# Optimization experiments

Hardware: AMD Instinct MI355X
Metric: run time of the kernel (lower is better)

Reference implementation:

```python
import jax, jax.numpy as jnp
import numpy as np

B, N, H_IN, H_HID, N_HEAD = 32, 500, 64, 16, 8
N_VALID = 400  # valid (non-padded) nodes per graph; node 0 is the root
NEG_INF = -1e20


def setup_inputs() -> dict:
    key = jax.random.key(0)
    ks = jax.random.split(key, 10)
    x = jax.random.normal(ks[0], (B, N, H_IN), jnp.float32)
    # sparse-ish binary adjacency with self loops
    A = (jax.random.uniform(ks[1], (B, N, N)) < 0.05).astype(jnp.float32)
    A = jnp.maximum(A, jnp.eye(N, dtype=jnp.float32)[None])
    # mask_nonzero: first N_VALID nodes of every graph are valid
    mask_batch = jnp.repeat(jnp.arange(B, dtype=jnp.int32), N_VALID)
    mask_row = jnp.tile(jnp.arange(N_VALID, dtype=jnp.int32), B)
    s = 0.1
    w1 = jax.random.normal(ks[2], (N_HEAD, H_IN, H_HID), jnp.float32) * s
    a_src1 = jax.random.normal(ks[3], (N_HEAD, H_HID), jnp.float32) * s
    a_dst1 = jax.random.normal(ks[4], (N_HEAD, H_HID), jnp.float32) * s
    w2 = jax.random.normal(ks[5], (1, N_HEAD * H_HID, H_IN), jnp.float32) * s
    a_src2 = jax.random.normal(ks[6], (1, H_IN), jnp.float32) * s
    a_dst2 = jax.random.normal(ks[7], (1, H_IN), jnp.float32) * s
    attn_w = jax.random.normal(ks[8], (2 * H_IN,), jnp.float32) * s
    return {"x": x, "A": A, "mask_batch": mask_batch, "mask_row": mask_row,
            "w1": w1, "a_src1": a_src1, "a_dst1": a_dst1,
            "w2": w2, "a_src2": a_src2, "a_dst2": a_dst2, "attn_w": attn_w}


def gat_layer(h_in, A, w, a_src, a_dst):
    # h_in: [B,N,F_in]; w: [H,F_in,F_out]
    h = jnp.einsum('bnf,hfo->bhno', h_in, w)              # [B,H,N,F_out]
    e_src = jnp.einsum('bhno,ho->bhn', h, a_src)          # [B,H,N]
    e_dst = jnp.einsum('bhno,ho->bhn', h, a_dst)
    e = jax.nn.leaky_relu(e_src[..., :, None] + e_dst[..., None, :], 0.2)  # [B,H,N,N]
    e = jnp.where(A[:, None, :, :] > 0, e, NEG_INF)
    attn = jax.nn.softmax(e, axis=-1)
    return jnp.einsum('bhnm,bhmo->bhno', attn, h)         # [B,H,N,F_out]


def reference(x, A, mask_batch, mask_row, w1, a_src1, a_dst1, w2, a_src2, a_dst2, attn_w):
    b, n, _ = x.shape
    # BatchGAT encoder: layer 1 (multi-head, concat + ELU), layer 2 (1 head -> h_in)
    h1 = gat_layer(x, A, w1, a_src1, a_dst1)                       # [B,H,N,h_hid]
    h1 = jax.nn.elu(h1).transpose(0, 2, 1, 3).reshape(b, n, -1)    # [B,N,H*h_hid]
    xc = gat_layer(h1, A, w2, a_src2, a_dst2)[:, 0]                # [B,N,h_in]
    # zero out padded nodes (so their Post_Attn scores are exactly 0)
    valid = jnp.zeros((b, n), x.dtype).at[mask_batch, mask_row].set(1.0)
    xc = xc * valid[:, :, None]
    # Post_Attn: scatter root features to each valid node position
    root = jnp.zeros_like(xc).at[mask_batch, mask_row, :].set(xc[mask_batch, 0, :])
    x_plus = jnp.concatenate([xc, root], axis=-1)                  # [B,N,2*h_in]
    score = x_plus @ attn_w                                        # [B,N]
    score = jnp.where(score == 0, NEG_INF, score)[:, :, None]      # masked_fill
    attn = jax.nn.softmax(score, axis=1)                           # softmax over nodes
    pooled = jnp.einsum('bnf,bn->bf', xc, attn[:, :, 0])           # [B,h_in]
    return pooled, attn
```

## Files before the change

### kernel.cpp

```cpp
#include <hip/hip_runtime.h>

#define NB 32
#define NN 500
#define HIN 64
#define HHID 16
#define NHEAD 8
#define NVALID 400
#define MAXK 128
#define NEG_INF -1e20f

__global__ __launch_bounds__(256) void k_nbr(const float* __restrict__ A,
                                             int* __restrict__ nbr, int* __restrict__ cnt)
{
    int row = blockIdx.x * 4 + (threadIdx.x >> 6);
    int lane = threadIdx.x & 63;
    if (row >= NB * NN) return;
    const float* arow = A + (size_t)row * NN;
    int c = 0;
    for (int it = 0; it < 8; ++it) {
        int m = it * 64 + lane;
        bool v = (m < NN) && (arow[m] > 0.0f);
        unsigned long long bal = __ballot(v);
        if (v) {
            int pos = c + __popcll(bal & ((1ull << lane) - 1ull));
            if (pos < MAXK) nbr[(size_t)row * MAXK + pos] = m;
        }
        c += (int)__popcll(bal);
    }
    if (lane == 0) cnt[row] = c < MAXK ? c : MAXK;
}

__global__ __launch_bounds__(256) void k_proj1(const float* __restrict__ x, const float* __restrict__ w1,
                                               const float* __restrict__ as1, const float* __restrict__ ad1,
                                               float* __restrict__ h1p, float* __restrict__ e1s,
                                               float* __restrict__ e1d)
{
    int b = blockIdx.y, chunk = blockIdx.x;
    int t = threadIdx.x, slot = t >> 7, lane = t & 127;
    int h = lane >> 4, o = lane & 15;
    float wreg[64];
#pragma unroll
    for (int f = 0; f < 64; ++f) wreg[f] = w1[h * 1024 + f * 16 + o];
    float as_r = as1[h * 16 + o], ad_r = ad1[h * 16 + o];
    __shared__ __align__(16) float xs[2][64];
    for (int i = 0; i < 8; ++i) {
        int n = chunk * 16 + i * 2 + slot;
        bool valid = n < NN;
        if (valid && lane < 64) xs[slot][lane] = x[(size_t)(b * NN + n) * HIN + lane];
        __syncthreads();
        if (valid) {
            float acc = 0.f;
#pragma unroll
            for (int f4 = 0; f4 < 16; ++f4) {
                float4 xv = *(const float4*)&xs[slot][f4 * 4];
                acc += xv.x * wreg[f4 * 4] + xv.y * wreg[f4 * 4 + 1]
                     + xv.z * wreg[f4 * 4 + 2] + xv.w * wreg[f4 * 4 + 3];
            }
            h1p[((size_t)(b * NHEAD + h) * NN + n) * HHID + o] = acc;
            float vs = acc * as_r, vd = acc * ad_r;
#pragma unroll
            for (int m = 1; m < 16; m <<= 1) { vs += __shfl_xor(vs, m); vd += __shfl_xor(vd, m); }
            if (o == 0) {
                e1s[(size_t)(b * NHEAD + h) * NN + n] = vs;
                e1d[(size_t)(b * NHEAD + h) * NN + n] = vd;
            }
        }
        __syncthreads();
    }
}

__global__ __launch_bounds__(128) void k_agg1(const int* __restrict__ nbr, const int* __restrict__ cnt,
                                              const float* __restrict__ h1p, const float* __restrict__ e1s,
                                              const float* __restrict__ e1d, float* __restrict__ h1cat)
{
    int row = blockIdx.x;
    int b = row / NN, n = row - b * NN;
    int t = threadIdx.x;
    __shared__ int nb_s[MAXK];
    __shared__ float p_s[NHEAD][MAXK];
    __shared__ float stat[NHEAD][2];
    int K = cnt[row];
    for (int k = t; k < K; k += 128) nb_s[k] = nbr[(size_t)row * MAXK + k];
    __syncthreads();
    for (int idx = t; idx < NHEAD * K; idx += 128) {
        int h = idx / K, k = idx - h * K;
        float e = e1s[(size_t)(b * NHEAD + h) * NN + n]
                + e1d[(size_t)(b * NHEAD + h) * NN + nb_s[k]];
        p_s[h][k] = e > 0.f ? e : 0.2f * e;
    }
    __syncthreads();
    if (t < NHEAD) {
        float mx = -1e30f;
        for (int k = 0; k < K; ++k) mx = fmaxf(mx, p_s[t][k]);
        float sum = 0.f;
        for (int k = 0; k < K; ++k) sum += __expf(p_s[t][k] - mx);
        stat[t][0] = mx; stat[t][1] = 1.f / sum;
    }
    __syncthreads();
    for (int idx = t; idx < NHEAD * K; idx += 128) {
        int h = idx / K, k = idx - h * K;
        p_s[h][k] = __expf(p_s[h][k] - stat[h][0]) * stat[h][1];
    }
    __syncthreads();
    int h = t >> 4, o = t & 15;
    float acc = 0.f;
    const float* hp = h1p + (size_t)(b * NHEAD + h) * NN * HHID + o;
    for (int k = 0; k < K; ++k) acc += p_s[h][k] * hp[(size_t)nb_s[k] * HHID];
    float outv = acc > 0.f ? acc : expm1f(acc);
    h1cat[(size_t)row * (NHEAD * HHID) + t] = outv;
}

__global__ __launch_bounds__(256) void k_proj2(const float* __restrict__ h1cat, const float* __restrict__ w2,
                                               const float* __restrict__ as2, const float* __restrict__ ad2,
                                               float* __restrict__ h2p, float* __restrict__ e2s,
                                               float* __restrict__ e2d)
{
    int b = blockIdx.y, chunk = blockIdx.x;
    int t = threadIdx.x, slot = t >> 7, lane = t & 127;
    int fh = lane >> 6, o = lane & 63;
    float wreg[64];
#pragma unroll
    for (int j = 0; j < 64; ++j) wreg[j] = w2[(fh * 64 + j) * 64 + o];
    float as_r = as2[o], ad_r = ad2[o];
    __shared__ __align__(16) float xs[2][128];
    __shared__ float part[2][128];
    for (int i = 0; i < 8; ++i) {
        int n = chunk * 16 + i * 2 + slot;
        bool valid = n < NN;
        if (valid) xs[slot][lane] = h1cat[(size_t)(b * NN + n) * 128 + lane];
        __syncthreads();
        float acc = 0.f;
        if (valid) {
#pragma unroll
            for (int j4 = 0; j4 < 16; ++j4) {
                float4 xv = *(const float4*)&xs[slot][fh * 64 + j4 * 4];
                acc += xv.x * wreg[j4 * 4] + xv.y * wreg[j4 * 4 + 1]
                     + xv.z * wreg[j4 * 4 + 2] + xv.w * wreg[j4 * 4 + 3];
            }
        }
        part[slot][lane] = acc;
        __syncthreads();
        if (valid && fh == 0) {
            float val = acc + part[slot][64 + o];
            h2p[(size_t)(b * NN + n) * 64 + o] = val;
            float vs = val * as_r, vd = val * ad_r;
#pragma unroll
            for (int m = 1; m < 64; m <<= 1) { vs += __shfl_xor(vs, m); vd += __shfl_xor(vd, m); }
            if (o == 0) { e2s[b * NN + n] = vs; e2d[b * NN + n] = vd; }
        }
        __syncthreads();
    }
}

__global__ __launch_bounds__(64) void k_agg2(const int* __restrict__ nbr, const int* __restrict__ cnt,
                                             const float* __restrict__ h2p, const float* __restrict__ e2s,
                                             const float* __restrict__ e2d, const float* __restrict__ aw,
                                             float* __restrict__ xc, float* __restrict__ sc,
                                             float* __restrict__ root_dot)
{
    int row = blockIdx.x;
    int b = row / NN, n = row - b * NN;
    int t = threadIdx.x;
    if (n >= NVALID) { xc[(size_t)row * 64 + t] = 0.f; return; }
    __shared__ int nb_s[MAXK];
    __shared__ float p_s[MAXK];
    __shared__ float stat[2];
    int K = cnt[row];
    for (int k = t; k < K; k += 64) nb_s[k] = nbr[(size_t)row * MAXK + k];
    __syncthreads();
    float es = e2s[row];
    for (int k = t; k < K; k += 64) {
        float e = es + e2d[b * NN + nb_s[k]];
        p_s[k] = e > 0.f ? e : 0.2f * e;
    }
    __syncthreads();
    if (t == 0) {
        float mx = -1e30f;
        for (int k = 0; k < K; ++k) mx = fmaxf(mx, p_s[k]);
        float sum = 0.f;
        for (int k = 0; k < K; ++k) sum += __expf(p_s[k] - mx);
        stat[0] = mx; stat[1] = 1.f / sum;
    }
    __syncthreads();
    for (int k = t; k < K; k += 64) p_s[k] = __expf(p_s[k] - stat[0]) * stat[1];
    __syncthreads();
    float acc = 0.f;
    for (int k = 0; k < K; ++k) acc += p_s[k] * h2p[(size_t)(b * NN + nb_s[k]) * 64 + t];
    xc[(size_t)row * 64 + t] = acc;
    float v = acc * aw[t];
#pragma unroll
    for (int m = 1; m < 64; m <<= 1) v += __shfl_xor(v, m);
    if (t == 0) sc[row] = v;
    if (n == 0) {
        float v2 = acc * aw[64 + t];
#pragma unroll
        for (int m = 1; m < 64; m <<= 1) v2 += __shfl_xor(v2, m);
        if (t == 0) root_dot[b] = v2;
    }
}

__global__ __launch_bounds__(1024) void k_pool(const float* __restrict__ xc, const float* __restrict__ sc,
                                               const float* __restrict__ root_dot, float* __restrict__ out)
{
    int b = blockIdx.x;
    int t = threadIdx.x, w = t >> 6, lane = t & 63;
    __shared__ float attn_s[NN];
    __shared__ float red[16];
    __shared__ float part[16][64];
    const float* xb = xc + (size_t)b * NN * 64;
    float rd = root_dot[b];
    float s = NEG_INF;
    if (t < NVALID) {
        s = sc[b * NN + t] + rd;
        if (s == 0.f) s = NEG_INF;
    }
    float mx = s;
#pragma unroll
    for (int m = 1; m < 64; m <<= 1) mx = fmaxf(mx, __shfl_xor(mx, m));
    if (lane == 0) red[w] = mx;
    __syncthreads();
    mx = red[0];
#pragma unroll
    for (int i = 1; i < 16; ++i) mx = fmaxf(mx, red[i]);
    float e = (t < NN) ? __expf(s - mx) : 0.f;
    float sum = e;
#pragma unroll
    for (int m = 1; m < 64; m <<= 1) sum += __shfl_xor(sum, m);
    __syncthreads();
    if (lane == 0) red[w] = sum;
    __syncthreads();
    sum = 0.f;
#pragma unroll
    for (int i = 0; i < 16; ++i) sum += red[i];
    float inv = 1.f / sum;
    if (t < NN) {
        float a = e * inv;
        out[NB * 64 + b * NN + t] = a;
        attn_s[t] = a;
    }
    __syncthreads();
    float acc = 0.f;
    for (int n = w; n < NN; n += 16) acc += attn_s[n] * xb[(size_t)n * 64 + lane];
    part[w][lane] = acc;
    __syncthreads();
    if (t < 64) {
        float v = 0.f;
#pragma unroll
        for (int i = 0; i < 16; ++i) v += part[i][t];
        out[b * 64 + t] = v;
    }
}

extern "C" void kernel_launch(void* const* d_in, const int* in_sizes, int n_in,
                              void* d_out, int out_size, void* d_ws, size_t ws_size,
                              hipStream_t stream) {
    const float* x   = (const float*)d_in[0];
    const float* A   = (const float*)d_in[1];
    const float* w1  = (const float*)d_in[4];
    const float* as1 = (const float*)d_in[5];
    const float* ad1 = (const float*)d_in[6];
    const float* w2  = (const float*)d_in[7];
    const float* as2 = (const float*)d_in[8];
    const float* ad2 = (const float*)d_in[9];
    const float* aw  = (const float*)d_in[10];
    float* out = (float*)d_out;

    char* ws = (char*)d_ws;
    int* nbr = (int*)ws;
    int* cnt = (int*)(ws + (size_t)16000 * 128 * 4);
    float* f = (float*)(ws + (size_t)16000 * 129 * 4);
    float* h1p   = f;  f += (size_t)NB * NHEAD * NN * HHID;
    float* e1s   = f;  f += (size_t)NB * NHEAD * NN;
    float* e1d   = f;  f += (size_t)NB * NHEAD * NN;
    float* h1cat = f;  f += (size_t)NB * NN * 128;
    float* h2p   = f;  f += (size_t)NB * NN * 64;
    float* e2s   = f;  f += (size_t)NB * NN;
    float* e2d   = f;  f += (size_t)NB * NN;
    float* xc    = f;  f += (size_t)NB * NN * 64;
    float* sc    = f;  f += (size_t)NB * NN;
    float* rootd = f;  f += NB;

    hipLaunchKernelGGL(k_nbr,   dim3(4000),   dim3(256), 0, stream, A, nbr, cnt);
    hipLaunchKernelGGL(k_proj1, dim3(32, NB), dim3(256), 0, stream, x, w1, as1, ad1, h1p, e1s, e1d);
    hipLaunchKernelGGL(k_agg1,  dim3(NB * NN), dim3(128), 0, stream, nbr, cnt, h1p, e1s, e1d, h1cat);
    hipLaunchKernelGGL(k_proj2, dim3(32, NB), dim3(256), 0, stream, h1cat, w2, as2, ad2, h2p, e2s, e2d);
    hipLaunchKernelGGL(k_agg2,  dim3(NB * NN), dim3(64), 0, stream, nbr, cnt, h2p, e2s, e2d, aw, xc, sc, rootd);
    hipLaunchKernelGGL(k_pool,  dim3(NB),     dim3(1024), 0, stream, xc, sc, rootd, out);
}
```

Baseline: 186.2 us.

## Fuse all six GAT stages into one cooperative persistent kernel with grid syncs

```diff
diff --git a/kernel.cpp b/kernel.cpp
--- a/kernel.cpp
+++ b/kernel.cpp
@@ -1,4 +1,7 @@
 #include <hip/hip_runtime.h>
+#include <hip/hip_cooperative_groups.h>
+
+namespace cg = cooperative_groups;
 
 #define NB 32
 #define NN 500
@@ -8,54 +11,69 @@
 #define NVALID 400
 #define MAXK 128
 #define NEG_INF -1e20f
-
-__global__ __launch_bounds__(256) void k_nbr(const float* __restrict__ A,
-                                             int* __restrict__ nbr, int* __restrict__ cnt)
+#define GRID 256
+#define BLK 512
+
+union SMem {
+    struct { int nb[8][MAXK]; float p[8][NHEAD][MAXK]; float inv[8][NHEAD]; } a1;
+    struct { int nb[8][MAXK]; float p[8][MAXK]; } a2;
+    struct { float attn[NN]; float red[8]; float part[8][64]; } pl;
+};
+
+__global__ __launch_bounds__(BLK, 2) void k_fused(
+    const float* __restrict__ x, const float* __restrict__ A,
+    const float* __restrict__ w1, const float* __restrict__ as1, const float* __restrict__ ad1,
+    const float* __restrict__ w2, const float* __restrict__ as2, const float* __restrict__ ad2,
+    const float* __restrict__ aw,
+    int* __restrict__ nbr, int* __restrict__ cnt,
+    float* __restrict__ h1p, float* __restrict__ e1s, float* __restrict__ e1d,
+    float* __restrict__ h1cat, float* __restrict__ h2p,
+    float* __restrict__ e2s, float* __restrict__ e2d,
+    float* __restrict__ xc, float* __restrict__ sc, float* __restrict__ rootd,
+    float* __restrict__ out)
 {
-    int row = blockIdx.x * 4 + (threadIdx.x >> 6);
-    int lane = threadIdx.x & 63;
-    if (row >= NB * NN) return;
-    const float* arow = A + (size_t)row * NN;
-    int c = 0;
-    for (int it = 0; it < 8; ++it) {
-        int m = it * 64 + lane;
-        bool v = (m < NN) && (arow[m] > 0.0f);
-        unsigned long long bal = __ballot(v);
-        if (v) {
-            int pos = c + __popcll(bal & ((1ull << lane) - 1ull));
-            if (pos < MAXK) nbr[(size_t)row * MAXK + pos] = m;
-        }
-        c += (int)__popcll(bal);
-    }
-    if (lane == 0) cnt[row] = c < MAXK ? c : MAXK;
-}
-
-__global__ __launch_bounds__(256) void k_proj1(const float* __restrict__ x, const float* __restrict__ w1,
-                                               const float* __restrict__ as1, const float* __restrict__ ad1,
-                                               float* __restrict__ h1p, float* __restrict__ e1s,
-                                               float* __restrict__ e1d)
-{
-    int b = blockIdx.y, chunk = blockIdx.x;
-    int t = threadIdx.x, slot = t >> 7, lane = t & 127;
-    int h = lane >> 4, o = lane & 15;
-    float wreg[64];
-#pragma unroll
-    for (int f = 0; f < 64; ++f) wreg[f] = w1[h * 1024 + f * 16 + o];
-    float as_r = as1[h * 16 + o], ad_r = ad1[h * 16 + o];
-    __shared__ __align__(16) float xs[2][64];
-    for (int i = 0; i < 8; ++i) {
-        int n = chunk * 16 + i * 2 + slot;
-        bool valid = n < NN;
-        if (valid && lane < 64) xs[slot][lane] = x[(size_t)(b * NN + n) * HIN + lane];
-        __syncthreads();
-        if (valid) {
-            float acc = 0.f;
-#pragma unroll
-            for (int f4 = 0; f4 < 16; ++f4) {
-                float4 xv = *(const float4*)&xs[slot][f4 * 4];
-                acc += xv.x * wreg[f4 * 4] + xv.y * wreg[f4 * 4 + 1]
-                     + xv.z * wreg[f4 * 4 + 2] + xv.w * wreg[f4 * 4 + 3];
-            }
+    cg::grid_group gg = cg::this_grid();
+    int t = threadIdx.x, wv = t >> 6, lane = t & 63;
+    __shared__ SMem sm;
+
+    for (int row = blockIdx.x * 8 + wv; row < NB * NN; row += GRID * 8) {
+        const float* ar = A + (size_t)row * NN;
+        int c = 0;
+        for (int it = 0; it < 8; ++it) {
+            int m = it * 64 + lane;
+            bool v = (m < NN) && (ar[m] > 0.f);
+            unsigned long long bal = __ballot(v);
+            if (v) {
+                int pos = c + __popcll(bal & ((1ull << lane) - 1ull));
+                if (pos < MAXK) nbr[(size_t)row * MAXK + pos] = m;
+            }
+            c += (int)__popcll(bal);
+        }
+        if (lane == 0) cnt[row] = c < MAXK ? c : MAXK;
+    }
+    gg.sync();
+
+    {
+        int g = t >> 7, gl = t & 127;
+        int unit = blockIdx.x * 4 + g;
+        int b = unit >> 5, chunk = unit & 31;
+        int h = (gl >> 4) & 7, o = gl & 15;
+        float wreg[64];
+#pragma unroll
+        for (int f = 0; f < 64; ++f) wreg[f] = w1[h * 1024 + f * 16 + o];
+        float as_r = as1[h * 16 + o], ad_r = ad1[h * 16 + o];
+        for (int i = 0; i < 16; ++i) {
+            int n = chunk * 16 + i;
+            if (n >= NN) break;
+            const float4* xp = (const float4*)(x + (size_t)(b * NN + n) * HIN);
+            float a0 = 0.f, a1 = 0.f;
+#pragma unroll
+            for (int f4 = 0; f4 < 16; f4 += 2) {
+                float4 u = xp[f4], v = xp[f4 + 1];
+                a0 += u.x * wreg[f4 * 4] + u.y * wreg[f4 * 4 + 1] + u.z * wreg[f4 * 4 + 2] + u.w * wreg[f4 * 4 + 3];
+                a1 += v.x * wreg[f4 * 4 + 4] + v.y * wreg[f4 * 4 + 5] + v.z * wreg[f4 * 4 + 6] + v.w * wreg[f4 * 4 + 7];
+            }
+            float acc = a0 + a1;
             h1p[((size_t)(b * NHEAD + h) * NN + n) * HHID + o] = acc;
             float vs = acc * as_r, vd = acc * ad_r;
 #pragma unroll
@@ -65,189 +83,184 @@
                 e1d[(size_t)(b * NHEAD + h) * NN + n] = vd;
             }
         }
-        __syncthreads();
-    }
-}
-
-__global__ __launch_bounds__(128) void k_agg1(const int* __restrict__ nbr, const int* __restrict__ cnt,
-                                              const float* __restrict__ h1p, const float* __restrict__ e1s,
-                                              const float* __restrict__ e1d, float* __restrict__ h1cat)
-{
-    int row = blockIdx.x;
-    int b = row / NN, n = row - b * NN;
-    int t = threadIdx.x;
-    __shared__ int nb_s[MAXK];
-    __shared__ float p_s[NHEAD][MAXK];
-    __shared__ float stat[NHEAD][2];
-    int K = cnt[row];
-    for (int k = t; k < K; k += 128) nb_s[k] = nbr[(size_t)row * MAXK + k];
-    __syncthreads();
-    for (int idx = t; idx < NHEAD * K; idx += 128) {
-        int h = idx / K, k = idx - h * K;
-        float e = e1s[(size_t)(b * NHEAD + h) * NN + n]
-                + e1d[(size_t)(b * NHEAD + h) * NN + nb_s[k]];
-        p_s[h][k] = e > 0.f ? e : 0.2f * e;
-    }
-    __syncthreads();
-    if (t < NHEAD) {
-        float mx = -1e30f;
-        for (int k = 0; k < K; ++k) mx = fmaxf(mx, p_s[t][k]);
-        float sum = 0.f;
-        for (int k = 0; k < K; ++k) sum += __expf(p_s[t][k] - mx);
-        stat[t][0] = mx; stat[t][1] = 1.f / sum;
-    }
-    __syncthreads();
-    for (int idx = t; idx < NHEAD * K; idx += 128) {
-        int h = idx / K, k = idx - h * K;
-        p_s[h][k] = __expf(p_s[h][k] - stat[h][0]) * stat[h][1];
-    }
-    __syncthreads();
-    int h = t >> 4, o = t & 15;
-    float acc = 0.f;
-    const float* hp = h1p + (size_t)(b * NHEAD + h) * NN * HHID + o;
-    for (int k = 0; k < K; ++k) acc += p_s[h][k] * hp[(size_t)nb_s[k] * HHID];
-    float outv = acc > 0.f ? acc : expm1f(acc);
-    h1cat[(size_t)row * (NHEAD * HHID) + t] = outv;
-}
-
-__global__ __launch_bounds__(256) void k_proj2(const float* __restrict__ h1cat, const float* __restrict__ w2,
-                                               const float* __restrict__ as2, const float* __restrict__ ad2,
-                                               float* __restrict__ h2p, float* __restrict__ e2s,
-                                               float* __restrict__ e2d)
-{
-    int b = blockIdx.y, chunk = blockIdx.x;
-    int t = threadIdx.x, slot = t >> 7, lane = t & 127;
-    int fh = lane >> 6, o = lane & 63;
-    float wreg[64];
-#pragma unroll
-    for (int j = 0; j < 64; ++j) wreg[j] = w2[(fh * 64 + j) * 64 + o];
-    float as_r = as2[o], ad_r = ad2[o];
-    __shared__ __align__(16) float xs[2][128];
-    __shared__ float part[2][128];
-    for (int i = 0; i < 8; ++i) {
-        int n = chunk * 16 + i * 2 + slot;
-        bool valid = n < NN;
-        if (valid) xs[slot][lane] = h1cat[(size_t)(b * NN + n) * 128 + lane];
-        __syncthreads();
+    }
+    gg.sync();
+
+    for (int row = blockIdx.x * 8 + wv; row < NB * NN; row += GRID * 8) {
+        int b = row / NN, n = row - b * NN;
+        int K = cnt[row];
+        for (int k = lane; k < K; k += 64) sm.a1.nb[wv][k] = nbr[(size_t)row * MAXK + k];
+        for (int h = 0; h < NHEAD; ++h) {
+            float es = e1s[(size_t)(b * NHEAD + h) * NN + n];
+            const float* ed = e1d + (size_t)(b * NHEAD + h) * NN;
+            float m = -1e30f;
+            for (int k = lane; k < K; k += 64) {
+                float e = es + ed[sm.a1.nb[wv][k]];
+                e = e > 0.f ? e : 0.2f * e;
+                sm.a1.p[wv][h][k] = e;
+                m = fmaxf(m, e);
+            }
+#pragma unroll
+            for (int mm = 1; mm < 64; mm <<= 1) m = fmaxf(m, __shfl_xor(m, mm));
+            float s = 0.f;
+            for (int k = lane; k < K; k += 64) {
+                float v = __expf(sm.a1.p[wv][h][k] - m);
+                sm.a1.p[wv][h][k] = v;
+                s += v;
+            }
+#pragma unroll
+            for (int mm = 1; mm < 64; mm <<= 1) s += __shfl_xor(s, mm);
+            if (lane == 0) sm.a1.inv[wv][h] = 1.f / s;
+        }
+#pragma unroll
+        for (int r = 0; r < 2; ++r) {
+            int oi = r * 64 + lane;
+            int h = oi >> 4, o = oi & 15;
+            const float* hp = h1p + (size_t)(b * NHEAD + h) * NN * HHID + o;
+            const float* pp = sm.a1.p[wv][h];
+            const int* nbp = sm.a1.nb[wv];
+            float acc = 0.f;
+            int k = 0;
+            for (; k + 4 <= K; k += 4) {
+                float p0 = pp[k], p1 = pp[k + 1], p2 = pp[k + 2], p3 = pp[k + 3];
+                int m0 = nbp[k], m1 = nbp[k + 1], m2 = nbp[k + 2], m3 = nbp[k + 3];
+                acc += p0 * hp[(size_t)m0 * HHID] + p1 * hp[(size_t)m1 * HHID]
+                     + p2 * hp[(size_t)m2 * HHID] + p3 * hp[(size_t)m3 * HHID];
+            }
+            for (; k < K; ++k) acc += pp[k] * hp[(size_t)nbp[k] * HHID];
+            acc *= sm.a1.inv[wv][h];
+            float v = acc > 0.f ? acc : expm1f(acc);
+            h1cat[(size_t)row * 128 + oi] = v;
+        }
+    }
+    gg.sync();
+
+    {
+        int g = t >> 7, gl = t & 127;
+        int unit = blockIdx.x * 4 + g;
+        int b = unit >> 5, chunk = unit & 31;
+        int s = gl >> 6, o = gl & 63;
+        float wreg2[128];
+#pragma unroll
+        for (int j = 0; j < 128; ++j) wreg2[j] = w2[j * 64 + o];
+        float as_r = as2[o], ad_r = ad2[o];
+        for (int i = 0; i < 8; ++i) {
+            int n = chunk * 16 + i * 2 + s;
+            if (n < NN) {
+                const float4* hp4 = (const float4*)(h1cat + (size_t)(b * NN + n) * 128);
+                float a0 = 0.f, a1 = 0.f, a2 = 0.f, a3 = 0.f;
+#pragma unroll
+                for (int j4 = 0; j4 < 32; j4 += 4) {
+                    float4 u0 = hp4[j4], u1 = hp4[j4 + 1], u2 = hp4[j4 + 2], u3 = hp4[j4 + 3];
+                    a0 += u0.x * wreg2[j4 * 4] + u0.y * wreg2[j4 * 4 + 1] + u0.z * wreg2[j4 * 4 + 2] + u0.w * wreg2[j4 * 4 + 3];
+                    a1 += u1.x * wreg2[j4 * 4 + 4] + u1.y * wreg2[j4 * 4 + 5] + u1.z * wreg2[j4 * 4 + 6] + u1.w * wreg2[j4 * 4 + 7];
+                    a2 += u2.x * wreg2[j4 * 4 + 8] + u2.y * wreg2[j4 * 4 + 9] + u2.z * wreg2[j4 * 4 + 10] + u2.w * wreg2[j4 * 4 + 11];
+                    a3 += u3.x * wreg2[j4 * 4 + 12] + u3.y * wreg2[j4 * 4 + 13] + u3.z * wreg2[j4 * 4 + 14] + u3.w * wreg2[j4 * 4 + 15];
+                }
+                float acc = (a0 + a1) + (a2 + a3);
+                h2p[(size_t)(b * NN + n) * 64 + o] = acc;
+                float vs = acc * as_r, vd = acc * ad_r;
+#pragma unroll
+                for (int m = 1; m < 64; m <<= 1) { vs += __shfl_xor(vs, m); vd += __shfl_xor(vd, m); }
+                if (o == 0) { e2s[b * NN + n] = vs; e2d[b * NN + n] = vd; }
+            }
+        }
+    }
+    gg.sync();
+
+    for (int row = blockIdx.x * 8 + wv; row < NB * NN; row += GRID * 8) {
+        int b = row / NN, n = row - b * NN;
+        if (n >= NVALID) { xc[(size_t)row * 64 + lane] = 0.f; continue; }
+        int K = cnt[row];
+        const int* nbg = nbr + (size_t)row * MAXK;
+        int i0 = (lane < K) ? nbg[lane] : 0;
+        int i1 = (lane + 64 < K) ? nbg[lane + 64] : 0;
+        sm.a2.nb[wv][lane] = i0; sm.a2.nb[wv][lane + 64] = i1;
+        float es = e2s[row];
+        const float* ed = e2d + b * NN;
+        float e0 = -1e30f, e1v = -1e30f;
+        if (lane < K)      { float e = es + ed[i0]; e0 = e > 0.f ? e : 0.2f * e; }
+        if (lane + 64 < K) { float e = es + ed[i1]; e1v = e > 0.f ? e : 0.2f * e; }
+        float m = fmaxf(e0, e1v);
+#pragma unroll
+        for (int mm = 1; mm < 64; mm <<= 1) m = fmaxf(m, __shfl_xor(m, mm));
+        float s0 = (lane < K) ? __expf(e0 - m) : 0.f;
+        float s1 = (lane + 64 < K) ? __expf(e1v - m) : 0.f;
+        float ss = s0 + s1;
+#pragma unroll
+        for (int mm = 1; mm < 64; mm <<= 1) ss += __shfl_xor(ss, mm);
+        float inv = 1.f / ss;
+        sm.a2.p[wv][lane] = s0 * inv; sm.a2.p[wv][lane + 64] = s1 * inv;
+        const float* h2b = h2p + (size_t)b * NN * 64 + lane;
+        const float* pp = sm.a2.p[wv];
+        const int* nbp = sm.a2.nb[wv];
         float acc = 0.f;
-        if (valid) {
-#pragma unroll
-            for (int j4 = 0; j4 < 16; ++j4) {
-                float4 xv = *(const float4*)&xs[slot][fh * 64 + j4 * 4];
-                acc += xv.x * wreg[j4 * 4] + xv.y * wreg[j4 * 4 + 1]
-                     + xv.z * wreg[j4 * 4 + 2] + xv.w * wreg[j4 * 4 + 3];
-            }
-        }
-        part[slot][lane] = acc;
-        __syncthreads();
-        if (valid && fh == 0) {
-            float val = acc + part[slot][64 + o];
-            h2p[(size_t)(b * NN + n) * 64 + o] = val;
-            float vs = val * as_r, vd = val * ad_r;
-#pragma unroll
-            for (int m = 1; m < 64; m <<= 1) { vs += __shfl_xor(vs, m); vd += __shfl_xor(vd, m); }
-            if (o == 0) { e2s[b * NN + n] = vs; e2d[b * NN + n] = vd; }
-        }
-        __syncthreads();
-    }
-}
-
-__global__ __launch_bounds__(64) void k_agg2(const int* __restrict__ nbr, const int* __restrict__ cnt,
-                                             const float* __restrict__ h2p, const float* __restrict__ e2s,
-                                             const float* __restrict__ e2d, const float* __restrict__ aw,
-                                             float* __restrict__ xc, float* __restrict__ sc,
-                                             float* __restrict__ root_dot)
-{
-    int row = blockIdx.x;
-    int b = row / NN, n = row - b * NN;
-    int t = threadIdx.x;
-    if (n >= NVALID) { xc[(size_t)row * 64 + t] = 0.f; return; }
-    __shared__ int nb_s[MAXK];
-    __shared__ float p_s[MAXK];
-    __shared__ float stat[2];
-    int K = cnt[row];
-    for (int k = t; k < K; k += 64) nb_s[k] = nbr[(size_t)row * MAXK + k];
-    __syncthreads();
-    float es = e2s[row];
-    for (int k = t; k < K; k += 64) {
-        float e = es + e2d[b * NN + nb_s[k]];
-        p_s[k] = e > 0.f ? e : 0.2f * e;
-    }
-    __syncthreads();
-    if (t == 0) {
-        float mx = -1e30f;
-        for (int k = 0; k < K; ++k) mx = fmaxf(mx, p_s[k]);
-        float sum = 0.f;
-        for (int k = 0; k < K; ++k) sum += __expf(p_s[k] - mx);
-        stat[0] = mx; stat[1] = 1.f / sum;
-    }
-    __syncthreads();
-    for (int k = t; k < K; k += 64) p_s[k] = __expf(p_s[k] - stat[0]) * stat[1];
-    __syncthreads();
-    float acc = 0.f;
-    for (int k = 0; k < K; ++k) acc += p_s[k] * h2p[(size_t)(b * NN + nb_s[k]) * 64 + t];
-    xc[(size_t)row * 64 + t] = acc;
-    float v = acc * aw[t];
-#pragma unroll
-    for (int m = 1; m < 64; m <<= 1) v += __shfl_xor(v, m);
-    if (t == 0) sc[row] = v;
-    if (n == 0) {
-        float v2 = acc * aw[64 + t];
-#pragma unroll
-        for (int m = 1; m < 64; m <<= 1) v2 += __shfl_xor(v2, m);
-        if (t == 0) root_dot[b] = v2;
-    }
-}
-
-__global__ __launch_bounds__(1024) void k_pool(const float* __restrict__ xc, const float* __restrict__ sc,
-                                               const float* __restrict__ root_dot, float* __restrict__ out)
-{
-    int b = blockIdx.x;
-    int t = threadIdx.x, w = t >> 6, lane = t & 63;
-    __shared__ float attn_s[NN];
-    __shared__ float red[16];
-    __shared__ float part[16][64];
-    const float* xb = xc + (size_t)b * NN * 64;
-    float rd = root_dot[b];
-    float s = NEG_INF;
-    if (t < NVALID) {
-        s = sc[b * NN + t] + rd;
-        if (s == 0.f) s = NEG_INF;
-    }
-    float mx = s;
-#pragma unroll
-    for (int m = 1; m < 64; m <<= 1) mx = fmaxf(mx, __shfl_xor(mx, m));
-    if (lane == 0) red[w] = mx;
-    __syncthreads();
-    mx = red[0];
-#pragma unroll
-    for (int i = 1; i < 16; ++i) mx = fmaxf(mx, red[i]);
-    float e = (t < NN) ? __expf(s - mx) : 0.f;
-    float sum = e;
-#pragma unroll
-    for (int m = 1; m < 64; m <<= 1) sum += __shfl_xor(sum, m);
-    __syncthreads();
-    if (lane == 0) red[w] = sum;
-    __syncthreads();
-    sum = 0.f;
-#pragma unroll
-    for (int i = 0; i < 16; ++i) sum += red[i];
-    float inv = 1.f / sum;
-    if (t < NN) {
-        float a = e * inv;
-        out[NB * 64 + b * NN + t] = a;
-        attn_s[t] = a;
-    }
-    __syncthreads();
-    float acc = 0.f;
-    for (int n = w; n < NN; n += 16) acc += attn_s[n] * xb[(size_t)n * 64 + lane];
-    part[w][lane] = acc;
-    __syncthreads();
-    if (t < 64) {
-        float v = 0.f;
-#pragma unroll
-        for (int i = 0; i < 16; ++i) v += part[i][t];
-        out[b * 64 + t] = v;
+        int k = 0;
+        for (; k + 4 <= K; k += 4) {
+            float p0 = pp[k], p1 = pp[k + 1], p2 = pp[k + 2], p3 = pp[k + 3];
+            int m0 = nbp[k], m1 = nbp[k + 1], m2 = nbp[k + 2], m3 = nbp[k + 3];
+            acc += p0 * h2b[(size_t)m0 * 64] + p1 * h2b[(size_t)m1 * 64]
+                 + p2 * h2b[(size_t)m2 * 64] + p3 * h2b[(size_t)m3 * 64];
+        }
+        for (; k < K; ++k) acc += pp[k] * h2b[(size_t)nbp[k] * 64];
+        xc[(size_t)row * 64 + lane] = acc;
+        float v = acc * aw[lane];
+#pragma unroll
+        for (int mm = 1; mm < 64; mm <<= 1) v += __shfl_xor(v, mm);
+        if (lane == 0) sc[row] = v;
+        if (n == 0) {
+            float v2 = acc * aw[64 + lane];
+#pragma unroll
+            for (int mm = 1; mm < 64; mm <<= 1) v2 += __shfl_xor(v2, mm);
+            if (lane == 0) rootd[b] = v2;
+        }
+    }
+    gg.sync();
+
+    if (blockIdx.x < NB) {
+        int b = blockIdx.x;
+        const float* xb = xc + (size_t)b * NN * 64;
+        float rd = rootd[b];
+        float s = NEG_INF;
+        if (t < NVALID) {
+            s = sc[b * NN + t] + rd;
+            if (s == 0.f) s = NEG_INF;
+        }
+        float mx = s;
+#pragma unroll
+        for (int mm = 1; mm < 64; mm <<= 1) mx = fmaxf(mx, __shfl_xor(mx, mm));
+        if (lane == 0) sm.pl.red[wv] = mx;
+        __syncthreads();
+        mx = sm.pl.red[0];
+#pragma unroll
+        for (int i = 1; i < 8; ++i) mx = fmaxf(mx, sm.pl.red[i]);
+        float e = (t < NN) ? __expf(s - mx) : 0.f;
+        float sum = e;
+#pragma unroll
+        for (int mm = 1; mm < 64; mm <<= 1) sum += __shfl_xor(sum, mm);
+        __syncthreads();
+        if (lane == 0) sm.pl.red[wv] = sum;
+        __syncthreads();
+        sum = 0.f;
+#pragma unroll
+        for (int i = 0; i < 8; ++i) sum += sm.pl.red[i];
+        float inv = 1.f / sum;
+        if (t < NN) {
+            float a = e * inv;
+            out[NB * HIN + b * NN + t] = a;
+            sm.pl.attn[t] = a;
+        }
+        __syncthreads();
+        float acc = 0.f;
+        for (int n2 = wv; n2 < NN; n2 += 8) acc += sm.pl.attn[n2] * xb[(size_t)n2 * 64 + lane];
+        sm.pl.part[wv][lane] = acc;
+        __syncthreads();
+        if (t < 64) {
+            float v = 0.f;
+#pragma unroll
+            for (int i = 0; i < 8; ++i) v += sm.pl.part[i][t];
+            out[b * 64 + t] = v;
+        }
     }
 }
 
@@ -280,10 +293,10 @@
     float* sc    = f;  f += (size_t)NB * NN;
     float* rootd = f;  f += NB;
 
-    hipLaunchKernelGGL(k_nbr,   dim3(4000),   dim3(256), 0, stream, A, nbr, cnt);
-    hipLaunchKernelGGL(k_proj1, dim3(32, NB), dim3(256), 0, stream, x, w1, as1, ad1, h1p, e1s, e1d);
-    hipLaunchKernelGGL(k_agg1,  dim3(NB * NN), dim3(128), 0, stream, nbr, cnt, h1p, e1s, e1d, h1cat);
-    hipLaunchKernelGGL(k_proj2, dim3(32, NB), dim3(256), 0, stream, h1cat, w2, as2, ad2, h2p, e2s, e2d);
-    hipLaunchKernelGGL(k_agg2,  dim3(NB * NN), dim3(64), 0, stream, nbr, cnt, h2p, e2s, e2d, aw, xc, sc, rootd);
-    hipLaunchKernelGGL(k_pool,  dim3(NB),     dim3(1024), 0, stream, xc, sc, rootd, out);
+    void* args[] = { (void*)&x, (void*)&A, (void*)&w1, (void*)&as1, (void*)&ad1,
+                     (void*)&w2, (void*)&as2, (void*)&ad2, (void*)&aw,
+                     (void*)&nbr, (void*)&cnt, (void*)&h1p, (void*)&e1s, (void*)&e1d,
+                     (void*)&h1cat, (void*)&h2p, (void*)&e2s, (void*)&e2d,
+                     (void*)&xc, (void*)&sc, (void*)&rootd, (void*)&out };
+    hipLaunchCooperativeKernel((const void*)k_fused, dim3(GRID), dim3(BLK), args, 0, stream);
 }
```

New measurement: 442.5 us. +137.6%, slower.

## Stage per-graph features in LDS and use wave-per-node GAT aggregation

Applied to the files above, without the earlier changes.

```diff
diff --git a/kernel.cpp b/kernel.cpp
--- a/kernel.cpp
+++ b/kernel.cpp
@@ -30,172 +30,212 @@
     if (lane == 0) cnt[row] = c < MAXK ? c : MAXK;
 }
 
-__global__ __launch_bounds__(256) void k_proj1(const float* __restrict__ x, const float* __restrict__ w1,
+__global__ __launch_bounds__(512) void k_proj1(const float* __restrict__ x, const float* __restrict__ w1,
                                                const float* __restrict__ as1, const float* __restrict__ ad1,
                                                float* __restrict__ h1p, float* __restrict__ e1s,
                                                float* __restrict__ e1d)
 {
-    int b = blockIdx.y, chunk = blockIdx.x;
-    int t = threadIdx.x, slot = t >> 7, lane = t & 127;
-    int h = lane >> 4, o = lane & 15;
-    float wreg[64];
-#pragma unroll
-    for (int f = 0; f < 64; ++f) wreg[f] = w1[h * 1024 + f * 16 + o];
-    float as_r = as1[h * 16 + o], ad_r = ad1[h * 16 + o];
-    __shared__ __align__(16) float xs[2][64];
-    for (int i = 0; i < 8; ++i) {
-        int n = chunk * 16 + i * 2 + slot;
-        bool valid = n < NN;
-        if (valid && lane < 64) xs[slot][lane] = x[(size_t)(b * NN + n) * HIN + lane];
-        __syncthreads();
-        if (valid) {
+    int t = threadIdx.x, wv = t >> 6, lane = t & 63;
+    __shared__ float w1s[8192];
+    for (int i = t; i < 8192; i += 512) {
+        int h = i >> 10, f = (i >> 4) & 63, o = i & 15;
+        w1s[f * 128 + h * 16 + o] = w1[i];
+    }
+    float as_r[2], ad_r[2];
+#pragma unroll
+    for (int rr = 0; rr < 2; ++rr) { as_r[rr] = as1[rr * 64 + lane]; ad_r[rr] = ad1[rr * 64 + lane]; }
+    __syncthreads();
+    int gw = blockIdx.x * 8 + wv;
+    for (int row = gw; row < NB * NN; row += 2000) {
+        const float4* xp4 = (const float4*)(x + (size_t)row * HIN);
+#pragma unroll
+        for (int rr = 0; rr < 2; ++rr) {
+            int oi = rr * 64 + lane;
+            const float* wp = w1s + oi;
             float acc = 0.f;
 #pragma unroll
             for (int f4 = 0; f4 < 16; ++f4) {
-                float4 xv = *(const float4*)&xs[slot][f4 * 4];
-                acc += xv.x * wreg[f4 * 4] + xv.y * wreg[f4 * 4 + 1]
-                     + xv.z * wreg[f4 * 4 + 2] + xv.w * wreg[f4 * 4 + 3];
+                float4 u = xp4[f4];
+                acc += u.x * wp[(f4 * 4 + 0) * 128] + u.y * wp[(f4 * 4 + 1) * 128]
+                     + u.z * wp[(f4 * 4 + 2) * 128] + u.w * wp[(f4 * 4 + 3) * 128];
             }
-            h1p[((size_t)(b * NHEAD + h) * NN + n) * HHID + o] = acc;
-            float vs = acc * as_r, vd = acc * ad_r;
+            h1p[(size_t)row * 128 + oi] = acc;
+            float vs = acc * as_r[rr], vd = acc * ad_r[rr];
 #pragma unroll
             for (int m = 1; m < 16; m <<= 1) { vs += __shfl_xor(vs, m); vd += __shfl_xor(vd, m); }
-            if (o == 0) {
-                e1s[(size_t)(b * NHEAD + h) * NN + n] = vs;
-                e1d[(size_t)(b * NHEAD + h) * NN + n] = vd;
+            if ((lane & 15) == 0) {
+                int h = oi >> 4;
+                e1s[(size_t)row * 8 + h] = vs;
+                e1d[(size_t)row * 8 + h] = vd;
             }
         }
-        __syncthreads();
-    }
-}
-
-__global__ __launch_bounds__(128) void k_agg1(const int* __restrict__ nbr, const int* __restrict__ cnt,
-                                              const float* __restrict__ h1p, const float* __restrict__ e1s,
-                                              const float* __restrict__ e1d, float* __restrict__ h1cat)
-{
-    int row = blockIdx.x;
-    int b = row / NN, n = row - b * NN;
-    int t = threadIdx.x;
-    __shared__ int nb_s[MAXK];
-    __shared__ float p_s[NHEAD][MAXK];
-    __shared__ float stat[NHEAD][2];
-    int K = cnt[row];
-    for (int k = t; k < K; k += 128) nb_s[k] = nbr[(size_t)row * MAXK + k];
-    __syncthreads();
-    for (int idx = t; idx < NHEAD * K; idx += 128) {
-        int h = idx / K, k = idx - h * K;
-        float e = e1s[(size_t)(b * NHEAD + h) * NN + n]
-                + e1d[(size_t)(b * NHEAD + h) * NN + nb_s[k]];
-        p_s[h][k] = e > 0.f ? e : 0.2f * e;
-    }
-    __syncthreads();
-    if (t < NHEAD) {
-        float mx = -1e30f;
-        for (int k = 0; k < K; ++k) mx = fmaxf(mx, p_s[t][k]);
-        float sum = 0.f;
-        for (int k = 0; k < K; ++k) sum += __expf(p_s[t][k] - mx);
-        stat[t][0] = mx; stat[t][1] = 1.f / sum;
-    }
-    __syncthreads();
-    for (int idx = t; idx < NHEAD * K; idx += 128) {
-        int h = idx / K, k = idx - h * K;
-        p_s[h][k] = __expf(p_s[h][k] - stat[h][0]) * stat[h][1];
-    }
-    __syncthreads();
-    int h = t >> 4, o = t & 15;
-    float acc = 0.f;
-    const float* hp = h1p + (size_t)(b * NHEAD + h) * NN * HHID + o;
-    for (int k = 0; k < K; ++k) acc += p_s[h][k] * hp[(size_t)nb_s[k] * HHID];
-    float outv = acc > 0.f ? acc : expm1f(acc);
-    h1cat[(size_t)row * (NHEAD * HHID) + t] = outv;
-}
-
-__global__ __launch_bounds__(256) void k_proj2(const float* __restrict__ h1cat, const float* __restrict__ w2,
+    }
+}
+
+__global__ __launch_bounds__(256, 1) void k_agg1(const int* __restrict__ nbr, const int* __restrict__ cnt,
+                                                 const float* __restrict__ h1p, const float* __restrict__ e1s,
+                                                 const float* __restrict__ e1d, float* __restrict__ h1cat)
+{
+    int rng = blockIdx.x, half = blockIdx.y, b = blockIdx.z;
+    int t = threadIdx.x, wv = t >> 6, lane = t & 63;
+    __shared__ __align__(16) float h1_s[NN][64];
+    __shared__ __align__(16) float e1s_s[NN][4];
+    __shared__ __align__(16) float e1d_s[NN][4];
+    __shared__ int   nb_s[4][MAXK];
+    __shared__ float p_s[4][4][132];
+    for (int i = t; i < NN * 16; i += 256) {
+        int n = i >> 4, f4 = i & 15;
+        ((float4*)h1_s[n])[f4] = ((const float4*)(h1p + (size_t)(b * NN + n) * 128 + half * 64))[f4];
+    }
+    for (int i = t; i < NN; i += 256) {
+        *(float4*)e1s_s[i] = *(const float4*)(e1s + (size_t)(b * NN + i) * 8 + half * 4);
+        *(float4*)e1d_s[i] = *(const float4*)(e1d + (size_t)(b * NN + i) * 8 + half * 4);
+    }
+    __syncthreads();
+    int n0 = rng * 125;
+    for (int n = n0 + wv; n < n0 + 125; n += 4) {
+        int row = b * NN + n;
+        int K = cnt[row];
+        const int* nbg = nbr + (size_t)row * MAXK;
+        int m0 = (lane < K) ? nbg[lane] : 0;
+        int m1 = (lane + 64 < K) ? nbg[lane + 64] : 0;
+        nb_s[wv][lane] = m0; nb_s[wv][lane + 64] = m1;
+        float4 es4 = *(const float4*)e1s_s[n];
+        float4 d0 = *(const float4*)e1d_s[m0];
+        float4 d1 = *(const float4*)e1d_s[m1];
+        float e0[4], e1v[4];
+        e0[0] = es4.x + d0.x; e0[1] = es4.y + d0.y; e0[2] = es4.z + d0.z; e0[3] = es4.w + d0.w;
+        e1v[0] = es4.x + d1.x; e1v[1] = es4.y + d1.y; e1v[2] = es4.z + d1.z; e1v[3] = es4.w + d1.w;
+#pragma unroll
+        for (int h = 0; h < 4; ++h) {
+            e0[h] = e0[h] > 0.f ? e0[h] : 0.2f * e0[h];
+            e1v[h] = e1v[h] > 0.f ? e1v[h] : 0.2f * e1v[h];
+            if (lane >= K) e0[h] = -1e30f;
+            if (lane + 64 >= K) e1v[h] = -1e30f;
+        }
+#pragma unroll
+        for (int h = 0; h < 4; ++h) {
+            float mx = fmaxf(e0[h], e1v[h]);
+#pragma unroll
+            for (int mm = 1; mm < 64; mm <<= 1) mx = fmaxf(mx, __shfl_xor(mx, mm));
+            float x0 = (lane < K) ? __expf(e0[h] - mx) : 0.f;
+            float x1 = (lane + 64 < K) ? __expf(e1v[h] - mx) : 0.f;
+            float s = x0 + x1;
+#pragma unroll
+            for (int mm = 1; mm < 64; mm <<= 1) s += __shfl_xor(s, mm);
+            float inv = 1.f / s;
+            p_s[wv][h][lane] = x0 * inv;
+            p_s[wv][h][lane + 64] = x1 * inv;
+        }
+        const float* pp = p_s[wv][lane >> 4];
+        const int* nbp = nb_s[wv];
+        float acc = 0.f;
+        int k = 0;
+        for (; k + 4 <= K; k += 4) {
+            float p0 = pp[k], p1 = pp[k + 1], p2 = pp[k + 2], p3 = pp[k + 3];
+            int q0 = nbp[k], q1 = nbp[k + 1], q2 = nbp[k + 2], q3 = nbp[k + 3];
+            acc += p0 * h1_s[q0][lane] + p1 * h1_s[q1][lane]
+                 + p2 * h1_s[q2][lane] + p3 * h1_s[q3][lane];
+        }
+        for (; k < K; ++k) acc += pp[k] * h1_s[nbp[k]][lane];
+        float v = acc > 0.f ? acc : expm1f(acc);
+        h1cat[(size_t)row * 128 + half * 64 + lane] = v;
+    }
+}
+
+__global__ __launch_bounds__(512) void k_proj2(const float* __restrict__ h1cat, const float* __restrict__ w2,
                                                const float* __restrict__ as2, const float* __restrict__ ad2,
                                                float* __restrict__ h2p, float* __restrict__ e2s,
                                                float* __restrict__ e2d)
 {
-    int b = blockIdx.y, chunk = blockIdx.x;
-    int t = threadIdx.x, slot = t >> 7, lane = t & 127;
-    int fh = lane >> 6, o = lane & 63;
-    float wreg[64];
-#pragma unroll
-    for (int j = 0; j < 64; ++j) wreg[j] = w2[(fh * 64 + j) * 64 + o];
-    float as_r = as2[o], ad_r = ad2[o];
-    __shared__ __align__(16) float xs[2][128];
-    __shared__ float part[2][128];
-    for (int i = 0; i < 8; ++i) {
-        int n = chunk * 16 + i * 2 + slot;
-        bool valid = n < NN;
-        if (valid) xs[slot][lane] = h1cat[(size_t)(b * NN + n) * 128 + lane];
-        __syncthreads();
+    int t = threadIdx.x, wv = t >> 6, lane = t & 63;
+    __shared__ float w2s[8192];
+    for (int i = t; i < 8192; i += 512) w2s[i] = w2[i];
+    float as_r = as2[lane], ad_r = ad2[lane];
+    __syncthreads();
+    int gw = blockIdx.x * 8 + wv;
+    for (int row = gw; row < NB * NN; row += 2000) {
+        const float4* hp4 = (const float4*)(h1cat + (size_t)row * 128);
+        const float* wp = w2s + lane;
         float acc = 0.f;
-        if (valid) {
-#pragma unroll
-            for (int j4 = 0; j4 < 16; ++j4) {
-                float4 xv = *(const float4*)&xs[slot][fh * 64 + j4 * 4];
-                acc += xv.x * wreg[j4 * 4] + xv.y * wreg[j4 * 4 + 1]
-                     + xv.z * wreg[j4 * 4 + 2] + xv.w * wreg[j4 * 4 + 3];
-            }
-        }
-        part[slot][lane] = acc;
-        __syncthreads();
-        if (valid && fh == 0) {
-            float val = acc + part[slot][64 + o];
-            h2p[(size_t)(b * NN + n) * 64 + o] = val;
-            float vs = val * as_r, vd = val * ad_r;
-#pragma unroll
-            for (int m = 1; m < 64; m <<= 1) { vs += __shfl_xor(vs, m); vd += __shfl_xor(vd, m); }
-            if (o == 0) { e2s[b * NN + n] = vs; e2d[b * NN + n] = vd; }
-        }
-        __syncthreads();
-    }
-}
-
-__global__ __launch_bounds__(64) void k_agg2(const int* __restrict__ nbr, const int* __restrict__ cnt,
-                                             const float* __restrict__ h2p, const float* __restrict__ e2s,
-                                             const float* __restrict__ e2d, const float* __restrict__ aw,
-                                             float* __restrict__ xc, float* __restrict__ sc,
-                                             float* __restrict__ root_dot)
-{
-    int row = blockIdx.x;
-    int b = row / NN, n = row - b * NN;
-    int t = threadIdx.x;
-    if (n >= NVALID) { xc[(size_t)row * 64 + t] = 0.f; return; }
-    __shared__ int nb_s[MAXK];
-    __shared__ float p_s[MAXK];
-    __shared__ float stat[2];
-    int K = cnt[row];
-    for (int k = t; k < K; k += 64) nb_s[k] = nbr[(size_t)row * MAXK + k];
-    __syncthreads();
-    float es = e2s[row];
-    for (int k = t; k < K; k += 64) {
-        float e = es + e2d[b * NN + nb_s[k]];
-        p_s[k] = e > 0.f ? e : 0.2f * e;
-    }
-    __syncthreads();
-    if (t == 0) {
-        float mx = -1e30f;
-        for (int k = 0; k < K; ++k) mx = fmaxf(mx, p_s[k]);
-        float sum = 0.f;
-        for (int k = 0; k < K; ++k) sum += __expf(p_s[k] - mx);
-        stat[0] = mx; stat[1] = 1.f / sum;
-    }
-    __syncthreads();
-    for (int k = t; k < K; k += 64) p_s[k] = __expf(p_s[k] - stat[0]) * stat[1];
-    __syncthreads();
-    float acc = 0.f;
-    for (int k = 0; k < K; ++k) acc += p_s[k] * h2p[(size_t)(b * NN + nb_s[k]) * 64 + t];
-    xc[(size_t)row * 64 + t] = acc;
-    float v = acc * aw[t];
-#pragma unroll
-    for (int m = 1; m < 64; m <<= 1) v += __shfl_xor(v, m);
-    if (t == 0) sc[row] = v;
-    if (n == 0) {
-        float v2 = acc * aw[64 + t];
-#pragma unroll
-        for (int m = 1; m < 64; m <<= 1) v2 += __shfl_xor(v2, m);
-        if (t == 0) root_dot[b] = v2;
+#pragma unroll 8
+        for (int j4 = 0; j4 < 32; ++j4) {
+            float4 u = hp4[j4];
+            acc += u.x * wp[(j4 * 4 + 0) * 64] + u.y * wp[(j4 * 4 + 1) * 64]
+                 + u.z * wp[(j4 * 4 + 2) * 64] + u.w * wp[(j4 * 4 + 3) * 64];
+        }
+        h2p[(size_t)row * 64 + lane] = acc;
+        float vs = acc * as_r, vd = acc * ad_r;
+#pragma unroll
+        for (int m = 1; m < 64; m <<= 1) { vs += __shfl_xor(vs, m); vd += __shfl_xor(vd, m); }
+        if (lane == 0) { e2s[row] = vs; e2d[row] = vd; }
+    }
+}
+
+__global__ __launch_bounds__(256, 1) void k_agg2(const int* __restrict__ nbr, const int* __restrict__ cnt,
+                                                 const float* __restrict__ h2p, const float* __restrict__ e2s,
+                                                 const float* __restrict__ e2d, const float* __restrict__ aw,
+                                                 float* __restrict__ xc, float* __restrict__ sc,
+                                                 float* __restrict__ rootd)
+{
+    int rng = blockIdx.x, b = blockIdx.y;
+    int t = threadIdx.x, wv = t >> 6, lane = t & 63;
+    __shared__ __align__(16) float h2_s[NN][64];
+    __shared__ float e2d_s[NN];
+    __shared__ int   nb_s[4][MAXK];
+    __shared__ float p_s[4][MAXK];
+    for (int i = t; i < NN * 16; i += 256) {
+        int n = i >> 4, f4 = i & 15;
+        ((float4*)h2_s[n])[f4] = ((const float4*)(h2p + (size_t)(b * NN + n) * 64))[f4];
+    }
+    for (int i = t; i < NN; i += 256) e2d_s[i] = e2d[b * NN + i];
+    __syncthreads();
+    float aw0 = aw[lane], aw64 = aw[64 + lane];
+    int n0 = rng * 63, n1 = n0 + 63 < NN ? n0 + 63 : NN;
+    for (int n = n0 + wv; n < n1; n += 4) {
+        int row = b * NN + n;
+        if (n >= NVALID) { xc[(size_t)row * 64 + lane] = 0.f; continue; }
+        int K = cnt[row];
+        const int* nbg = nbr + (size_t)row * MAXK;
+        int m0 = (lane < K) ? nbg[lane] : 0;
+        int m1 = (lane + 64 < K) ? nbg[lane + 64] : 0;
+        nb_s[wv][lane] = m0; nb_s[wv][lane + 64] = m1;
+        float es = e2s[row];
+        float e0 = -1e30f, e1v = -1e30f;
+        if (lane < K)      { float e = es + e2d_s[m0]; e0 = e > 0.f ? e : 0.2f * e; }
+        if (lane + 64 < K) { float e = es + e2d_s[m1]; e1v = e > 0.f ? e : 0.2f * e; }
+        float mx = fmaxf(e0, e1v);
+#pragma unroll
+        for (int mm = 1; mm < 64; mm <<= 1) mx = fmaxf(mx, __shfl_xor(mx, mm));
+        float x0 = (lane < K) ? __expf(e0 - mx) : 0.f;
+        float x1 = (lane + 64 < K) ? __expf(e1v - mx) : 0.f;
+        float ss = x0 + x1;
+#pragma unroll
+        for (int mm = 1; mm < 64; mm <<= 1) ss += __shfl_xor(ss, mm);
+        float inv = 1.f / ss;
+        p_s[wv][lane] = x0 * inv; p_s[wv][lane + 64] = x1 * inv;
+        const float* pp = p_s[wv];
+        const int* nbp = nb_s[wv];
+        float acc = 0.f;
+        int k = 0;
+        for (; k + 4 <= K; k += 4) {
+            float p0 = pp[k], p1 = pp[k + 1], p2 = pp[k + 2], p3 = pp[k + 3];
+            int q0 = nbp[k], q1 = nbp[k + 1], q2 = nbp[k + 2], q3 = nbp[k + 3];
+            acc += p0 * h2_s[q0][lane] + p1 * h2_s[q1][lane]
+                 + p2 * h2_s[q2][lane] + p3 * h2_s[q3][lane];
+        }
+        for (; k < K; ++k) acc += pp[k] * h2_s[nbp[k]][lane];
+        xc[(size_t)row * 64 + lane] = acc;
+        float v = acc * aw0;
+#pragma unroll
+        for (int mm = 1; mm < 64; mm <<= 1) v += __shfl_xor(v, mm);
+        if (lane == 0) sc[row] = v;
+        if (n == 0) {
+            float v2 = acc * aw64;
+#pragma unroll
+            for (int mm = 1; mm < 64; mm <<= 1) v2 += __shfl_xor(v2, mm);
+            if (lane == 0) rootd[b] = v2;
+        }
     }
 }
 
@@ -269,9 +309,9 @@
     int* nbr = (int*)ws;
     int* cnt = (int*)(ws + (size_t)16000 * 128 * 4);
     float* f = (float*)(ws + (size_t)16000 * 129 * 4);
-    float* h1p   = f;  f += (size_t)NB * NHEAD * NN * HHID;
-    float* e1s   = f;  f += (size_t)NB * NHEAD * NN;
-    float* e1d   = f;  f += (size_t)NB * NHEAD * NN;
+    float* h1p   = f;  f += (size_t)NB * NN * 128;
+    float* e1s   = f;  f += (size_t)NB * NN * 8;
+    float* e1d   = f;  f += (size_t)NB * NN * 8;
     float* h1cat = f;  f += (size_t)NB * NN * 128;
     float* h2p   = f;  f += (size_t)NB * NN * 64;
     float* e2s   = f;  f += (size_t)NB * NN;
@@ -280,10 +320,10 @@
     float* sc    = f;  f += (size_t)NB * NN;
     float* rootd = f;  f += NB;
 
-    hipLaunchKernelGGL(k_nbr,   dim3(4000),   dim3(256), 0, stream, A, nbr, cnt);
-    hipLaunchKernelGGL(k_proj1, dim3(32, NB), dim3(256), 0, stream, x, w1, as1, ad1, h1p, e1s, e1d);
-    hipLaunchKernelGGL(k_agg1,  dim3(NB * NN), dim3(128), 0, stream, nbr, cnt, h1p, e1s, e1d, h1cat);
-    hipLaunchKernelGGL(k_proj2, dim3(32, NB), dim3(256), 0, stream, h1cat, w2, as2, ad2, h2p, e2s, e2d);
-    hipLaunchKernelGGL(k_agg2,  dim3(NB * NN), dim3(64), 0, stream, nbr, cnt, h2p, e2s, e2d, aw, xc, sc, rootd);
-    hipLaunchKernelGGL(k_pool,  dim3(NB),     dim3(1024), 0, stream, xc, sc, rootd, out);
-}
+    hipLaunchKernelGGL(k_nbr,   dim3(4000),        dim3(256),  0, stream, A, nbr, cnt);
+    hipLaunchKernelGGL(k_proj1, dim3(250),         dim3(512),  0, stream, x, w1, as1, ad1, h1p, e1s, e1d);
+    hipLaunchKernelGGL(k_agg1,  dim3(4, 2, NB),    dim3(256),  0, stream, nbr, cnt, h1p, e1s, e1d, h1cat);
+    hipLaunchKernelGGL(k_proj2, dim3(250),         dim3(512),  0, stream, h1cat, w2, as2, ad2, h2p, e2s, e2d);
+    hipLaunchKernelGGL(k_agg2,  dim3(8, NB),       dim3(256),  0, stream, nbr, cnt, h2p, e2s, e2d, aw, xc, sc, rootd);
+    hipLaunchKernelGGL(k_pool,  dim3(NB),          dim3(1024), 0, stream, xc, sc, rootd, out);
+}
```

After: 293.3 us. +57.5%, slower.
